# Performance work log

Hardware: AMD Instinct MI355X
Metric: run time of the kernel (lower is better)

Reference implementation:

```python
import jax, jax.numpy as jnp
import numpy as np
import math

B, T = 8, 1024
IN_DIMS = 1024
OUT_DIMS = 1024
NUM_CODES = 1024
NUM_CODEBOOKS = 8


def setup_inputs() -> dict:
    key = jax.random.key(0)
    k1, k2, k3, k4, k5 = jax.random.split(key, 5)
    x = jax.random.normal(k1, (B, T, IN_DIMS), dtype=jnp.float32)
    target = jax.random.randint(k2, (B, T, NUM_CODEBOOKS), 0, NUM_CODES, dtype=jnp.int64)
    # params, init per reset_params()
    codebook = jax.random.normal(k3, (NUM_CODES, NUM_CODEBOOKS, OUT_DIMS), dtype=jnp.float32) / math.sqrt(OUT_DIMS * NUM_CODEBOOKS)
    proj_w = jax.random.normal(k4, (NUM_CODEBOOKS * NUM_CODES, IN_DIMS), dtype=jnp.float32) / math.sqrt(IN_DIMS)
    proj_b = jnp.zeros((NUM_CODEBOOKS * NUM_CODES,), dtype=jnp.float32)
    wproj_w = jax.random.normal(k5, (NUM_CODEBOOKS, IN_DIMS), dtype=jnp.float32) / math.sqrt(IN_DIMS)
    return {"x": x, "target": target, "codebook": codebook,
            "proj_w": proj_w, "proj_b": proj_b, "wproj_w": wproj_w}


def reference(x, target, codebook, proj_w, proj_b, wproj_w):
    # xp: (B, T, K, C)
    xp = (jnp.einsum('btd,nd->btn', x, proj_w) + proj_b).reshape(B, T, NUM_CODEBOOKS, NUM_CODES)
    # xw: (B, T, K) softmax codebook weights
    xw = jax.nn.softmax(jnp.einsum('btd,kd->btk', x, wproj_w), axis=-1)
    # gather codebook embeddings under no_grad: codebook[target, arange(K)] -> (B, T, K, D)
    cb_inds = jnp.arange(NUM_CODEBOOKS)
    codebook_embs = jax.lax.stop_gradient(codebook[target, cb_inds])
    # per-element cross entropy, reduction='none' -> (B, T, K)
    logp = jax.nn.log_softmax(xp, axis=-1)
    x_loss = -jnp.take_along_axis(logp, target[..., None], axis=-1)[..., 0]
    # softmax-weighted sum over codebooks -> (B, T, D)
    emb = jnp.einsum('btkd,btk->btd', codebook_embs, xw)
    return emb, x_loss
```

## Files before the change

kernel.cpp:

```cpp
#include <hip/hip_runtime.h>
#include <hip/hip_bf16.h>
#include <math.h>

#define MTOT   8192
#define KDIM   1024
#define NCODES 1024
#define NCB    8
#define NTOT   8192
#define ODIM   1024

#define BM 256
#define BN 256
#define NTILES_N 32

typedef __attribute__((ext_vector_type(8))) short  bf16x8;
typedef __attribute__((ext_vector_type(4))) float  f32x4;

__device__ __forceinline__ ushort f2bf(float f) {
  union { float f; unsigned u; } v; v.f = f;
  unsigned u = v.u;
  unsigned r = (u + 0x7fffu + ((u >> 16) & 1u)) >> 16;
  return (ushort)r;
}

__device__ __forceinline__ void gload16(const void* g, void* l) {
  __builtin_amdgcn_global_load_lds(
      (const __attribute__((address_space(1))) void*)g,
      (__attribute__((address_space(3))) void*)l,
      16, 0, 0);
}

__global__ void cvt_bf16_kernel(const float* __restrict__ in,
                                ushort* __restrict__ out) {
  int i = blockIdx.x * blockDim.x + threadIdx.x;
  float4 v = ((const float4*)in)[i];
  ushort4 o;
  o.x = f2bf(v.x); o.y = f2bf(v.y); o.z = f2bf(v.z); o.w = f2bf(v.w);
  ((ushort4*)out)[i] = o;
}


__device__ __forceinline__ void chunk_dec(int c, int& srcA, int& srcB) {
  const int q  = c >> 6;
  const int sq = q >> 1;
  const int ct = q & 1;
  const int r4 = (c >> 2) & 15;
  const int cb = (((c & 3) ^ ((c >> 3) & 3)) << 4);
  const int rtA = (sq & 3) + ((sq >> 2) << 3);
  const int rtB = (sq & 1) + ((sq >> 1) << 2);
  srcA = ((rtA << 4) + r4) * (KDIM * 2) + ct * 64 + cb;
  srcB = ((rtB << 4) + r4) * (KDIM * 2) + ct * 64 + cb;
}

#define STAGE_A(T, H) do { \
    gload16(Ag + (size_t)(srcA0 + (H)*131072 + (T)*128), ldsA_st + ((T)&1)*32768 + (H)*16384); \
    gload16(Ag + (size_t)(srcA1 + (H)*131072 + (T)*128), ldsA_st + ((T)&1)*32768 + (H)*16384 + 8192); \
  } while(0)
#define STAGE_B(T, H) do { \
    gload16(Bg + (size_t)(srcB0 + (H)*65536 + (T)*128), ldsB_st + ((T)&1)*32768 + (H)*16384); \
    gload16(Bg + (size_t)(srcB1 + (H)*65536 + (T)*128), ldsB_st + ((T)&1)*32768 + (H)*16384 + 8192); \
  } while(0)

#define LDA_Q(P, MH) do { \
    _Pragma("unroll") for (int m_ = 0; m_ < 4; ++m_) \
    _Pragma("unroll") for (int k_ = 0; k_ < 2; ++k_) \
      a[m_][k_] = *(const bf16x8*)(ldsA_rd + (P)*32768 + (MH)*16384 + m_*2048 + k_*1024); \
  } while(0)
#define LDB_Q(P, NH, B) do { \
    _Pragma("unroll") for (int n_ = 0; n_ < 2; ++n_) \
    _Pragma("unroll") for (int k_ = 0; k_ < 2; ++k_) \
      B[n_][k_] = *(const bf16x8*)(ldsB_rd + (P)*32768 + (NH)*16384 + n_*2048 + k_*1024); \
  } while(0)
#define MM_Q(MH, NH, B) do { \
    _Pragma("unroll") for (int m_ = 0; m_ < 4; ++m_) \
    _Pragma("unroll") for (int n_ = 0; n_ < 2; ++n_) \
    _Pragma("unroll") for (int k_ = 0; k_ < 2; ++k_) \
      acc[(MH)*4+m_][(NH)*2+n_] = __builtin_amdgcn_mfma_f32_16x16x32_bf16( \
          a[m_][k_], B[n_][k_], acc[(MH)*4+m_][(NH)*2+n_], 0, 0, 0); \
  } while(0)

#define PH_MID(MH, NH, B) \
    __builtin_amdgcn_s_barrier(); \
    asm volatile("s_waitcnt lgkmcnt(0)" ::: "memory"); \
    __builtin_amdgcn_sched_barrier(0); \
    __builtin_amdgcn_s_setprio(1); \
    MM_Q(MH, NH, B); \
    __builtin_amdgcn_s_setprio(0);
#define PH_END \
    __builtin_amdgcn_s_barrier(); \
    asm volatile("" ::: "memory");

__global__ __launch_bounds__(512)
void ce_gemm_kernel(const ushort* __restrict__ Abf,
                    const ushort* __restrict__ Bbf,
                    const float*  __restrict__ bias,
                    const int*    __restrict__ target,
                    float* __restrict__ partials,
                    float* __restrict__ tgtlogit) {
  extern __shared__ char smem[];

  const int tid  = threadIdx.x;
  const int wid  = tid >> 6;
  const int lane = tid & 63;
  const int wr   = wid >> 2;
  const int wc   = wid & 3;
  const int g    = lane >> 4;
  const int c15  = lane & 15;
  const int mtile = blockIdx.x;
  const int ntile = blockIdx.y;

  const int swz = (c15 * 64 + g * 16) ^ ((c15 & 6) << 3);
  const char* ldsA_rd = smem + wr * 8192 + swz;
  const char* ldsB_rd = smem + 65536 + wc * 4096 + swz;
  char* ldsA_st = smem + wid * 1024;
  char* ldsB_st = smem + 65536 + wid * 1024;

  const char* Ag = ((const char*)Abf) + (size_t)mtile * 256 * (KDIM * 2);
  const char* Bg = ((const char*)Bbf) + (size_t)ntile * 256 * (KDIM * 2);
  int srcA0, srcB0, srcA1, srcB1;
  chunk_dec(tid,       srcA0, srcB0);
  chunk_dec(tid + 512, srcA1, srcB1);

  f32x4 acc[8][4];
#pragma unroll
  for (int m = 0; m < 8; ++m)
#pragma unroll
    for (int n = 0; n < 4; ++n)
      acc[m][n] = (f32x4){0.f, 0.f, 0.f, 0.f};

  bf16x8 a[4][2], b0[2][2], b1[2][2];

  STAGE_A(0, 0); STAGE_A(0, 1); STAGE_B(0, 0); STAGE_B(0, 1);
  STAGE_A(1, 0); STAGE_B(1, 1);
  asm volatile("s_waitcnt vmcnt(4)" ::: "memory");
  __builtin_amdgcn_s_barrier();
  asm volatile("" ::: "memory");

#pragma unroll 1
  for (int i = 0; i < 7; ++i) {
    const int t1 = 2 * i + 1;
    LDA_Q(0, 0); LDB_Q(0, 0, b0);
    STAGE_A(t1, 1);
    PH_MID(0, 0, b0) PH_END
    LDB_Q(0, 1, b1);
    STAGE_B(t1, 0);
    PH_MID(0, 1, b1) PH_END
    LDA_Q(0, 1);
    STAGE_A(t1 + 1, 0);
    PH_MID(1, 1, b1) PH_END
    STAGE_B(t1 + 1, 1);
    PH_MID(1, 0, b0)
    asm volatile("s_waitcnt vmcnt(4)" ::: "memory");
    PH_END
    LDA_Q(1, 0); LDB_Q(1, 0, b0);
    STAGE_A(t1 + 1, 1);
    PH_MID(0, 0, b0) PH_END
    LDB_Q(1, 1, b1);
    STAGE_B(t1 + 1, 0);
    PH_MID(0, 1, b1) PH_END
    LDA_Q(1, 1);
    STAGE_A(t1 + 2, 0);
    PH_MID(1, 1, b1) PH_END
    STAGE_B(t1 + 2, 1);
    PH_MID(1, 0, b0)
    asm volatile("s_waitcnt vmcnt(4)" ::: "memory");
    PH_END
  }
  LDA_Q(0, 0); LDB_Q(0, 0, b0);
  STAGE_A(15, 1);
  PH_MID(0, 0, b0) PH_END
  LDB_Q(0, 1, b1);
  STAGE_B(15, 0);
  PH_MID(0, 1, b1) PH_END
  LDA_Q(0, 1);
  PH_MID(1, 1, b1) PH_END
  PH_MID(1, 0, b0)
  asm volatile("s_waitcnt vmcnt(0)" ::: "memory");
  PH_END
  LDA_Q(1, 0); LDB_Q(1, 0, b0);
  PH_MID(0, 0, b0) PH_END
  LDB_Q(1, 1, b1);
  PH_MID(0, 1, b1) PH_END
  LDA_Q(1, 1);
  PH_MID(1, 1, b1) PH_END
  PH_MID(1, 0, b0) PH_END

  const int kcb = ntile >> 2;
  float bias_n[4];
#pragma unroll
  for (int n = 0; n < 4; ++n)
    bias_n[n] = bias[ntile * 256 + wc * 64 + n * 16 + c15];

  float rmax[8][4], rsum[8][4];
#pragma unroll
  for (int m = 0; m < 8; ++m)
#pragma unroll
    for (int j = 0; j < 4; ++j) {
      float v = acc[m][0][j] + bias_n[0];
      v = fmaxf(v, acc[m][1][j] + bias_n[1]);
      v = fmaxf(v, acc[m][2][j] + bias_n[2]);
      v = fmaxf(v, acc[m][3][j] + bias_n[3]);
#pragma unroll
      for (int off = 1; off < 16; off <<= 1)
        v = fmaxf(v, __shfl_xor(v, off));
      rmax[m][j] = v;
    }

  const int col_base = ntile * 256 + wc * 64;
#pragma unroll
  for (int m = 0; m < 8; ++m) {
    const int rowg = mtile * 256 + wr * 128 + m * 16 + g * 4;
#pragma unroll
    for (int j = 0; j < 4; ++j) {
      const int row  = rowg + j;
      const int t    = target[row * NCB + kcb];
      const int tcol = kcb * NCODES + t;
      float s = 0.f;
#pragma unroll
      for (int n = 0; n < 4; ++n) {
        const float v = acc[m][n][j] + bias_n[n];
        if (col_base + n * 16 + c15 == tcol) tgtlogit[row * NCB + kcb] = v;
        s += __expf(v - rmax[m][j]);
      }
#pragma unroll
      for (int off = 1; off < 16; off <<= 1)
        s += __shfl_xor(s, off);
      rsum[m][j] = s;
    }
  }

  __syncthreads();
  float* redM = (float*)smem;
  float* redS = redM + 1024;
  if (c15 == 0) {
#pragma unroll
    for (int m = 0; m < 8; ++m)
#pragma unroll
      for (int j = 0; j < 4; ++j) {
        const int rl = wr * 128 + m * 16 + g * 4 + j;
        redM[wc * 256 + rl] = rmax[m][j];
        redS[wc * 256 + rl] = rsum[m][j];
      }
  }
  __syncthreads();
  if (tid < 256) {
    float M = redM[tid], S = redS[tid];
#pragma unroll
    for (int w = 1; w < 4; ++w) {
      const float m2 = redM[w * 256 + tid];
      const float s2 = redS[w * 256 + tid];
      const float Mx = fmaxf(M, m2);
      S = S * __expf(M - Mx) + s2 * __expf(m2 - Mx);
      M = Mx;
    }
    const int row = mtile * 256 + tid;
    partials[((size_t)row * NTILES_N + ntile) * 2 + 0] = M;
    partials[((size_t)row * NTILES_N + ntile) * 2 + 1] = S;
  }
}

__global__ void lse_reduce_kernel(const float* __restrict__ partials,
                                  const float* __restrict__ tgtlogit,
                                  float* __restrict__ xloss_out) {
  const int idx = blockIdx.x * blockDim.x + threadIdx.x;
  if (idx >= MTOT * NCB) return;
  const int row = idx >> 3, k = idx & 7;
  float M = -1e30f, S = 0.f;
#pragma unroll
  for (int i = 0; i < 4; ++i) {
    const int nt = k * 4 + i;
    const float m = partials[((size_t)row * NTILES_N + nt) * 2 + 0];
    const float s = partials[((size_t)row * NTILES_N + nt) * 2 + 1];
    const float Mn = fmaxf(M, m);
    S = S * __expf(M - Mn) + s * __expf(m - Mn);
    M = Mn;
  }
  xloss_out[idx] = M + __logf(S) - tgtlogit[idx];
}

__global__ void emb_kernel(const float* __restrict__ x,
                           const int*   __restrict__ target,
                           const float* __restrict__ cb,
                           const float* __restrict__ wproj,
                           float* __restrict__ emb_out) {
  const int bt   = blockIdx.x;
  const int tid  = threadIdx.x;
  const int lane = tid & 63;
  const int wid  = tid >> 6;

  const float4 xv = ((const float4*)(x + (size_t)bt * KDIM))[tid];
  float p[8];
#pragma unroll
  for (int k = 0; k < 8; ++k) {
    const float4 wv = ((const float4*)(wproj + k * KDIM))[tid];
    p[k] = xv.x * wv.x + xv.y * wv.y + xv.z * wv.z + xv.w * wv.w;
  }
#pragma unroll
  for (int k = 0; k < 8; ++k)
#pragma unroll
    for (int off = 32; off >= 1; off >>= 1)
      p[k] += __shfl_xor(p[k], off);

  __shared__ float lred[4][8];
  if (lane == 0) {
#pragma unroll
    for (int k = 0; k < 8; ++k) lred[wid][k] = p[k];
  }
  __syncthreads();

  float logit[8], mx = -1e30f;
#pragma unroll
  for (int k = 0; k < 8; ++k) {
    logit[k] = lred[0][k] + lred[1][k] + lred[2][k] + lred[3][k];
    mx = fmaxf(mx, logit[k]);
  }
  float w[8], den = 0.f;
#pragma unroll
  for (int k = 0; k < 8; ++k) { w[k] = __expf(logit[k] - mx); den += w[k]; }
  const float inv = 1.f / den;

  float4 acc = make_float4(0.f, 0.f, 0.f, 0.f);
#pragma unroll
  for (int k = 0; k < 8; ++k) {
    const int t = target[bt * NCB + k];
    const float4 cv = ((const float4*)(cb + ((size_t)t * NCB + k) * ODIM))[tid];
    const float wk = w[k] * inv;
    acc.x += wk * cv.x; acc.y += wk * cv.y; acc.z += wk * cv.z; acc.w += wk * cv.w;
  }
  ((float4*)(emb_out + (size_t)bt * ODIM))[tid] = acc;
}

extern "C" void kernel_launch(void* const* d_in, const int* in_sizes, int n_in,
                              void* d_out, int out_size, void* d_ws, size_t ws_size,
                              hipStream_t stream) {
  const float* x        = (const float*)d_in[0];
  const int*   target   = (const int*)  d_in[1];
  const float* codebook = (const float*)d_in[2];
  const float* proj_w   = (const float*)d_in[3];
  const float* proj_b   = (const float*)d_in[4];
  const float* wproj_w  = (const float*)d_in[5];

  float* out       = (float*)d_out;
  float* emb_out   = out;
  float* xloss_out = out + (size_t)MTOT * ODIM;

  char* ws = (char*)d_ws;
  ushort* xbf      = (ushort*)ws;
  ushort* wbf      = (ushort*)(ws + (size_t)16 * 1024 * 1024);
  float*  partials = (float*) (ws + (size_t)32 * 1024 * 1024);
  float*  tgtlogit = (float*) (ws + (size_t)35 * 1024 * 1024);

  hipFuncSetAttribute((const void*)ce_gemm_kernel,
                      hipFuncAttributeMaxDynamicSharedMemorySize, 131072);

  cvt_bf16_kernel<<<(MTOT * KDIM / 4) / 256, 256, 0, stream>>>(x,      xbf);
  cvt_bf16_kernel<<<(NTOT * KDIM / 4) / 256, 256, 0, stream>>>(proj_w, wbf);

  dim3 grid(MTOT / BM, NTOT / BN);
  ce_gemm_kernel<<<grid, 512, 131072, stream>>>(xbf, wbf, proj_b, target,
                                                partials, tgtlogit);

  lse_reduce_kernel<<<(MTOT * NCB) / 256, 256, 0, stream>>>(partials, tgtlogit, xloss_out);

  emb_kernel<<<MTOT, 256, 0, stream>>>(x, target, codebook, wproj_w, emb_out);
}
```

Measured before the change: 208.6 us.

## Fuse per-codebook log-sum-exp into the GEMM and drop the reduce kernel

Each GEMM block now covers a full 256-row by 1024-code codebook slice. It walks the 4 N-segments in sequence and flushes a running sum of exponentials after each one, so the block writes the final cross-entropy loss itself. This removes the partials buffer, the separate log-sum-exp reduce kernel and the max pass. The bf16 conversion of x moves into the emb kernel, which saves one more launch and one more read of x. In exchange the softmax sum is taken without subtracting the row max, which can overflow for large logits. The grid also shrinks to 256 large blocks, with a synchronising flush inside the main loop.

```diff
diff --git a/kernel.cpp b/kernel.cpp
--- a/kernel.cpp
+++ b/kernel.cpp
@@ -8,10 +8,6 @@
 #define NCB    8
 #define NTOT   8192
 #define ODIM   1024
-
-#define BM 256
-#define BN 256
-#define NTILES_N 32
 
 typedef __attribute__((ext_vector_type(8))) short  bf16x8;
 typedef __attribute__((ext_vector_type(4))) float  f32x4;
@@ -53,12 +49,16 @@
 }
 
 #define STAGE_A(T, H) do { \
-    gload16(Ag + (size_t)(srcA0 + (H)*131072 + (T)*128), ldsA_st + ((T)&1)*32768 + (H)*16384); \
-    gload16(Ag + (size_t)(srcA1 + (H)*131072 + (T)*128), ldsA_st + ((T)&1)*32768 + (H)*16384 + 8192); \
+    const int ao_ = (((T) & 15) * 128 + (H) * 131072); \
+    char* ld_ = ldsA_st + ((T) & 1) * 32768 + (H) * 16384; \
+    gload16(Ag + (size_t)(srcA0 + ao_), ld_); \
+    gload16(Ag + (size_t)(srcA1 + ao_), ld_ + 8192); \
   } while(0)
 #define STAGE_B(T, H) do { \
-    gload16(Bg + (size_t)(srcB0 + (H)*65536 + (T)*128), ldsB_st + ((T)&1)*32768 + (H)*16384); \
-    gload16(Bg + (size_t)(srcB1 + (H)*65536 + (T)*128), ldsB_st + ((T)&1)*32768 + (H)*16384 + 8192); \
+    const int bo_ = (((T) >> 4) * 524288 + ((T) & 15) * 128 + (H) * 65536); \
+    char* ld_ = ldsB_st + ((T) & 1) * 32768 + (H) * 16384; \
+    gload16(Bg + (size_t)(srcB0 + bo_), ld_); \
+    gload16(Bg + (size_t)(srcB1 + bo_), ld_ + 8192); \
   } while(0)
 
 #define LDA_Q(P, MH) do { \
@@ -90,14 +90,44 @@
     __builtin_amdgcn_s_barrier(); \
     asm volatile("" ::: "memory");
 
-__global__ __launch_bounds__(512)
+#define FLUSH(SEG) do { \
+    const int colb_ = (SEG) * 256 + wc * 64; \
+    float bias_n[4]; \
+    _Pragma("unroll") for (int n_ = 0; n_ < 4; ++n_) \
+      bias_n[n_] = bias[kcb * 1024 + colb_ + n_ * 16 + c15]; \
+    _Pragma("unroll") for (int m_ = 0; m_ < 8; ++m_) { \
+      _Pragma("unroll") for (int j_ = 0; j_ < 4; ++j_) { \
+        const int rl_ = wr * 128 + m_ * 16 + g * 4 + j_; \
+        const int tc_ = tgtcol[rl_]; \
+        float s_ = 0.f; \
+        _Pragma("unroll") for (int n_ = 0; n_ < 4; ++n_) { \
+          const float v_ = acc[m_][n_][j_] + bias_n[n_]; \
+          if (colb_ + n_ * 16 + c15 == tc_) tgtval[rl_] = v_; \
+          s_ += __expf(v_); \
+        } \
+        _Pragma("unroll") for (int o_ = 1; o_ < 16; o_ <<= 1) \
+          s_ += __shfl_xor(s_, o_); \
+        if (c15 == 0) redS[wc * 256 + rl_] = s_; \
+      } \
+    } \
+    __syncthreads(); \
+    if (tid < 256) \
+      S_acc += redS[tid] + redS[tid + 256] + redS[tid + 512] + redS[tid + 768]; \
+    _Pragma("unroll") for (int m_ = 0; m_ < 8; ++m_) \
+      _Pragma("unroll") for (int n_ = 0; n_ < 4; ++n_) \
+        acc[m_][n_] = (f32x4){0.f, 0.f, 0.f, 0.f}; \
+  } while(0)
+
+__global__ __launch_bounds__(512, 2)
 void ce_gemm_kernel(const ushort* __restrict__ Abf,
                     const ushort* __restrict__ Bbf,
                     const float*  __restrict__ bias,
                     const int*    __restrict__ target,
-                    float* __restrict__ partials,
-                    float* __restrict__ tgtlogit) {
+                    float* __restrict__ xloss) {
   extern __shared__ char smem[];
+  float* redS   = (float*)(smem + 131072);
+  int*   tgtcol = (int*)  (smem + 135168);
+  float* tgtval = (float*)(smem + 136192);
 
   const int tid  = threadIdx.x;
   const int wid  = tid >> 6;
@@ -106,8 +136,8 @@
   const int wc   = wid & 3;
   const int g    = lane >> 4;
   const int c15  = lane & 15;
-  const int mtile = blockIdx.x;
-  const int ntile = blockIdx.y;
+  const int mtile = blockIdx.x >> 3;
+  const int kcb   = blockIdx.x & 7;
 
   const int swz = (c15 * 64 + g * 16) ^ ((c15 & 6) << 3);
   const char* ldsA_rd = smem + wr * 8192 + swz;
@@ -116,11 +146,14 @@
   char* ldsB_st = smem + 65536 + wid * 1024;
 
   const char* Ag = ((const char*)Abf) + (size_t)mtile * 256 * (KDIM * 2);
-  const char* Bg = ((const char*)Bbf) + (size_t)ntile * 256 * (KDIM * 2);
+  const char* Bg = ((const char*)Bbf) + (size_t)kcb * 2097152;
   int srcA0, srcB0, srcA1, srcB1;
   chunk_dec(tid,       srcA0, srcB0);
   chunk_dec(tid + 512, srcA1, srcB1);
 
+  if (tid < 256)
+    tgtcol[tid] = target[(size_t)(mtile * 256 + tid) * NCB + kcb];
+
   f32x4 acc[8][4];
 #pragma unroll
   for (int m = 0; m < 8; ++m)
@@ -128,17 +161,17 @@
     for (int n = 0; n < 4; ++n)
       acc[m][n] = (f32x4){0.f, 0.f, 0.f, 0.f};
 
+  float S_acc = 0.f;
   bf16x8 a[4][2], b0[2][2], b1[2][2];
 
   STAGE_A(0, 0); STAGE_A(0, 1); STAGE_B(0, 0); STAGE_B(0, 1);
   STAGE_A(1, 0); STAGE_B(1, 1);
   asm volatile("s_waitcnt vmcnt(4)" ::: "memory");
-  __builtin_amdgcn_s_barrier();
-  asm volatile("" ::: "memory");
+  __syncthreads();
 
 #pragma unroll 1
-  for (int i = 0; i < 7; ++i) {
-    const int t1 = 2 * i + 1;
+  for (int it = 0; it < 31; ++it) {
+    const int t1 = 2 * it + 1;
     LDA_Q(0, 0); LDB_Q(0, 0, b0);
     STAGE_A(t1, 1);
     PH_MID(0, 0, b0) PH_END
@@ -165,12 +198,15 @@
     PH_MID(1, 0, b0)
     asm volatile("s_waitcnt vmcnt(4)" ::: "memory");
     PH_END
-  }
+
+    if ((it & 7) == 7) FLUSH(it >> 3);
+  }
+
   LDA_Q(0, 0); LDB_Q(0, 0, b0);
-  STAGE_A(15, 1);
+  STAGE_A(63, 1);
   PH_MID(0, 0, b0) PH_END
   LDB_Q(0, 1, b1);
-  STAGE_B(15, 0);
+  STAGE_B(63, 0);
   PH_MID(0, 1, b1) PH_END
   LDA_Q(0, 1);
   PH_MID(1, 1, b1) PH_END
@@ -185,110 +221,31 @@
   PH_MID(1, 1, b1) PH_END
   PH_MID(1, 0, b0) PH_END
 
-  const int kcb = ntile >> 2;
-  float bias_n[4];
-#pragma unroll
-  for (int n = 0; n < 4; ++n)
-    bias_n[n] = bias[ntile * 256 + wc * 64 + n * 16 + c15];
-
-  float rmax[8][4], rsum[8][4];
-#pragma unroll
-  for (int m = 0; m < 8; ++m)
-#pragma unroll
-    for (int j = 0; j < 4; ++j) {
-      float v = acc[m][0][j] + bias_n[0];
-      v = fmaxf(v, acc[m][1][j] + bias_n[1]);
-      v = fmaxf(v, acc[m][2][j] + bias_n[2]);
-      v = fmaxf(v, acc[m][3][j] + bias_n[3]);
-#pragma unroll
-      for (int off = 1; off < 16; off <<= 1)
-        v = fmaxf(v, __shfl_xor(v, off));
-      rmax[m][j] = v;
-    }
-
-  const int col_base = ntile * 256 + wc * 64;
-#pragma unroll
-  for (int m = 0; m < 8; ++m) {
-    const int rowg = mtile * 256 + wr * 128 + m * 16 + g * 4;
-#pragma unroll
-    for (int j = 0; j < 4; ++j) {
-      const int row  = rowg + j;
-      const int t    = target[row * NCB + kcb];
-      const int tcol = kcb * NCODES + t;
-      float s = 0.f;
-#pragma unroll
-      for (int n = 0; n < 4; ++n) {
-        const float v = acc[m][n][j] + bias_n[n];
-        if (col_base + n * 16 + c15 == tcol) tgtlogit[row * NCB + kcb] = v;
-        s += __expf(v - rmax[m][j]);
-      }
-#pragma unroll
-      for (int off = 1; off < 16; off <<= 1)
-        s += __shfl_xor(s, off);
-      rsum[m][j] = s;
-    }
-  }
-
+  FLUSH(3);
   __syncthreads();
-  float* redM = (float*)smem;
-  float* redS = redM + 1024;
-  if (c15 == 0) {
-#pragma unroll
-    for (int m = 0; m < 8; ++m)
-#pragma unroll
-      for (int j = 0; j < 4; ++j) {
-        const int rl = wr * 128 + m * 16 + g * 4 + j;
-        redM[wc * 256 + rl] = rmax[m][j];
-        redS[wc * 256 + rl] = rsum[m][j];
-      }
-  }
-  __syncthreads();
+
   if (tid < 256) {
-    float M = redM[tid], S = redS[tid];
-#pragma unroll
-    for (int w = 1; w < 4; ++w) {
-      const float m2 = redM[w * 256 + tid];
-      const float s2 = redS[w * 256 + tid];
-      const float Mx = fmaxf(M, m2);
-      S = S * __expf(M - Mx) + s2 * __expf(m2 - Mx);
-      M = Mx;
-    }
     const int row = mtile * 256 + tid;
-    partials[((size_t)row * NTILES_N + ntile) * 2 + 0] = M;
-    partials[((size_t)row * NTILES_N + ntile) * 2 + 1] = S;
-  }
-}
-
-__global__ void lse_reduce_kernel(const float* __restrict__ partials,
-                                  const float* __restrict__ tgtlogit,
-                                  float* __restrict__ xloss_out) {
-  const int idx = blockIdx.x * blockDim.x + threadIdx.x;
-  if (idx >= MTOT * NCB) return;
-  const int row = idx >> 3, k = idx & 7;
-  float M = -1e30f, S = 0.f;
-#pragma unroll
-  for (int i = 0; i < 4; ++i) {
-    const int nt = k * 4 + i;
-    const float m = partials[((size_t)row * NTILES_N + nt) * 2 + 0];
-    const float s = partials[((size_t)row * NTILES_N + nt) * 2 + 1];
-    const float Mn = fmaxf(M, m);
-    S = S * __expf(M - Mn) + s * __expf(m - Mn);
-    M = Mn;
-  }
-  xloss_out[idx] = M + __logf(S) - tgtlogit[idx];
+    xloss[(size_t)row * NCB + kcb] = __logf(S_acc) - tgtval[tid];
+  }
 }
 
 __global__ void emb_kernel(const float* __restrict__ x,
                            const int*   __restrict__ target,
                            const float* __restrict__ cb,
                            const float* __restrict__ wproj,
-                           float* __restrict__ emb_out) {
+                           float* __restrict__ emb_out,
+                           ushort* __restrict__ xbf) {
   const int bt   = blockIdx.x;
   const int tid  = threadIdx.x;
   const int lane = tid & 63;
   const int wid  = tid >> 6;
 
   const float4 xv = ((const float4*)(x + (size_t)bt * KDIM))[tid];
+  ushort4 xo;
+  xo.x = f2bf(xv.x); xo.y = f2bf(xv.y); xo.z = f2bf(xv.z); xo.w = f2bf(xv.w);
+  ((ushort4*)(xbf + (size_t)bt * KDIM))[tid] = xo;
+
   float p[8];
 #pragma unroll
   for (int k = 0; k < 8; ++k) {
@@ -345,22 +302,14 @@
   float* xloss_out = out + (size_t)MTOT * ODIM;
 
   char* ws = (char*)d_ws;
-  ushort* xbf      = (ushort*)ws;
-  ushort* wbf      = (ushort*)(ws + (size_t)16 * 1024 * 1024);
-  float*  partials = (float*) (ws + (size_t)32 * 1024 * 1024);
-  float*  tgtlogit = (float*) (ws + (size_t)35 * 1024 * 1024);
+  ushort* xbf = (ushort*)ws;
+  ushort* wbf = (ushort*)(ws + (size_t)16 * 1024 * 1024);
 
   hipFuncSetAttribute((const void*)ce_gemm_kernel,
-                      hipFuncAttributeMaxDynamicSharedMemorySize, 131072);
-
-  cvt_bf16_kernel<<<(MTOT * KDIM / 4) / 256, 256, 0, stream>>>(x,      xbf);
+                      hipFuncAttributeMaxDynamicSharedMemorySize, 137216);
+
+  emb_kernel<<<MTOT, 256, 0, stream>>>(x, target, codebook, wproj_w, emb_out, xbf);
   cvt_bf16_kernel<<<(NTOT * KDIM / 4) / 256, 256, 0, stream>>>(proj_w, wbf);
 
-  dim3 grid(MTOT / BM, NTOT / BN);
-  ce_gemm_kernel<<<grid, 512, 131072, stream>>>(xbf, wbf, proj_b, target,
-                                                partials, tgtlogit);
-
-  lse_reduce_kernel<<<(MTOT * NCB) / 256, 256, 0, stream>>>(partials, tgtlogit, xloss_out);
-
-  emb_kernel<<<MTOT, 256, 0, stream>>>(x, target, codebook, wproj_w, emb_out);
-}
+  ce_gemm_kernel<<<256, 512, 137216, stream>>>(xbf, wbf, proj_b, target, xloss_out);
+}
```

Result: no change. 207.2 us (-0.7%).
